# Performance work log

Measured on AMD Instinct MI355X. Metric: run time of the kernel, lower is better.

Reference implementation:

```python
import jax, jax.numpy as jnp
import numpy as np

B, N, H, W = 64, 32, 200, 200


def setup_inputs() -> dict:
    key = jax.random.key(0)
    k1, k2, k3, k4 = jax.random.split(key, 4)
    return {
        "parameter": jax.random.uniform(k1, (B, N, 3), dtype=jnp.float32),
        "x_start": jax.random.uniform(k2, (), dtype=jnp.float32),
        "y_start": jax.random.uniform(k3, (), dtype=jnp.float32),
        "theta": jax.random.uniform(k4, (), dtype=jnp.float32, minval=-3.14159, maxval=3.14159),
        # learned parameters at their torch init values
        "weights": jnp.eye(2, dtype=jnp.float32),
        "biases": jnp.zeros(2, dtype=jnp.float32),
        "thick_mult": jnp.array(0.5, dtype=jnp.float32),
        "thick_bias": jnp.array(0.1, dtype=jnp.float32),
        "dark_exp": jnp.array(1.0, dtype=jnp.float32),
        "dark_non_lin_weight": jnp.array(0.5, dtype=jnp.float32),
        "x_m": jnp.array(1.0, dtype=jnp.float32),
        "y_m": jnp.array(1.0, dtype=jnp.float32),
        "x_b": jnp.array(0.0, dtype=jnp.float32),
        "y_b": jnp.array(0.0, dtype=jnp.float32),
        "use_conv": 0,
    }


def reference(parameter, x_start, y_start, theta, weights, biases, thick_mult,
              thick_bias, dark_exp, dark_non_lin_weight, x_m, y_m, x_b, y_b,
              use_conv):
    # torch.flip(traj, dims=(2,)) then traj[:,:,0] *= -1:
    # channel0 (y) = -parameter[...,1], channel1 (x) = parameter[...,0]
    y0 = -parameter[..., 1]
    x0 = parameter[..., 0]
    # rotation about origin (vectorized over batch; identical per-element math)
    c, s = jnp.cos(theta), jnp.sin(theta)
    x_rot = x0 * c + y0 * s
    y_rot = -x0 * s + y0 * c
    yy = y_rot * y_m + y_b + y_start
    xx = x_rot * x_m + x_b + x_start
    traj = jnp.stack([yy, xx], axis=-1)                      # (B,N,2)
    # curve_to_stroke: matmul(weights, curve).T + biases == traj @ weights.T + biases
    strokes = traj @ weights.T + biases                      # (B,N,2)
    thick = (parameter[..., 2] * 2.0 + 0.5) / 64.0           # (B,N)
    # grid_coords: channel0 = row/H, channel1 = col/W
    gy = jnp.arange(H, dtype=strokes.dtype) / H
    gx = jnp.arange(W, dtype=strokes.dtype) / W
    coords = jnp.stack(jnp.meshgrid(gy, gx, indexing='ij'), axis=-1)  # (H,W,2)
    v = strokes[:, :-1, None, None, :]                       # (B,N-1,1,1,2)
    w = strokes[:, 1:, None, None, :]
    p = coords[None, None]                                   # (1,1,H,W,2)
    wv = w - v
    d2 = jnp.sum(wv * wv, axis=-1)                           # (B,N-1,1,1)
    dot = jnp.sum((p - v) * wv, axis=-1) / (d2 + 1e-5)       # (B,N-1,H,W)
    frac = jnp.clip(dot, 0.0, 1.0)
    proj = v + frac[..., None] * wv                          # (B,N-1,H,W,2)
    diff = p - proj
    dist = jnp.sqrt(jnp.sum(diff * diff, axis=-1))           # (B,N-1,H,W)
    th = thick[:, :-1, None, None] * (1.0 - frac) + thick[:, 1:, None, None] * frac
    th = jnp.maximum(th * thick_mult + thick_bias, 1e-8)
    dark = jnp.clip((th - dist) / th, 0.0, 1.0)
    dark = (dark + 1e-4) ** dark_exp
    nl = jax.nn.sigmoid(dark * 16.0 - 8.0)
    dark = dark_non_lin_weight * nl + (1.0 - dark_non_lin_weight) * dark
    return jnp.max(dark, axis=1)                             # (B,H,W)
```

## Files before the change

kernel.cpp:

```cpp
#include <hip/hip_runtime.h>
#include <math.h>

#define B_ 64
#define N_ 32
#define H_ 200
#define W_ 200
#define NSEG (N_ - 1)
#define TS 32
#define NT 7
#define TILE_RAD 0.111f

__global__ __launch_bounds__(256) void stroke_kernel(
    const float* __restrict__ param,
    const float* __restrict__ x_start,
    const float* __restrict__ y_start,
    const float* __restrict__ theta,
    const float* __restrict__ weights,
    const float* __restrict__ biases,
    const float* __restrict__ thick_mult,
    const float* __restrict__ thick_bias,
    const float* __restrict__ dark_exp_p,
    const float* __restrict__ dark_nlw_p,
    const float* __restrict__ x_m_p,
    const float* __restrict__ y_m_p,
    const float* __restrict__ x_b_p,
    const float* __restrict__ y_b_p,
    float* __restrict__ out)
{
    __shared__ float4 s_A[NSEG];
    __shared__ float4 s_B[NSEG];

    const int b    = blockIdx.z;
    const int tid  = threadIdx.x;
    const int lane = tid & 63;

    const float dexp = dark_exp_p[0], dnlw = dark_nlw_p[0];

    float sy = 0.0f, sx = 0.0f, tk = 0.0f;
    const float tm = thick_mult[0], tb = thick_bias[0];
    if (lane < N_) {
        const float thv = theta[0];
        const float c   = __cosf(thv), s = __sinf(thv);
        const float xs  = x_start[0], ys = y_start[0];
        const float W00 = weights[0], W01 = weights[1];
        const float W10 = weights[2], W11 = weights[3];
        const float bb0 = biases[0],  bb1 = biases[1];
        const float xm  = x_m_p[0], ym = y_m_p[0];
        const float xb  = x_b_p[0], yb = y_b_p[0];
        float p0 = param[(b * N_ + lane) * 3 + 0];
        float p1 = param[(b * N_ + lane) * 3 + 1];
        float p2 = param[(b * N_ + lane) * 3 + 2];
        float x0 = p0, y0 = -p1;
        float x_rot =  x0 * c + y0 * s;
        float y_rot = -x0 * s + y0 * c;
        float yy = y_rot * ym + yb + ys;
        float xx = x_rot * xm + xb + xs;
        sy = yy * W00 + xx * W01 + bb0;
        sx = yy * W10 + xx * W11 + bb1;
        tk = (p2 * 2.0f + 0.5f) * (1.0f / 64.0f);
    }
    float sy1 = __shfl_down(sy, 1);
    float sx1 = __shfl_down(sx, 1);
    float tk1 = __shfl_down(tk, 1);

    bool keep = false;
    float4 A4 = make_float4(0,0,0,0), B4 = make_float4(0,0,0,0);
    if (lane < NSEG) {
        float wvy = sy1 - sy, wvx = sx1 - sx;
        float d2 = wvy * wvy + wvx * wvx;
        float inv_d2 = 1.0f / (d2 + 1e-5f);
        float c0 = tk * tm + tb;
        float c1 = (tk1 - tk) * tm;
        A4 = make_float4(sy, sx, wvy, wvx);
        B4 = make_float4(inv_d2, c0, c1, wvx * inv_d2 * (1.0f / W_));
        const float cy = ((float)(blockIdx.y * TS) + 15.5f) * (1.0f / H_);
        const float cx = ((float)(blockIdx.x * TS) + 15.5f) * (1.0f / W_);
        float dyc = cy - sy, dxc = cx - sx;
        float dot = (dyc * wvy + dxc * wvx) * inv_d2;
        float fr  = __builtin_amdgcn_fmed3f(dot, 0.0f, 1.0f);
        float ey  = dyc - fr * wvy;
        float ex  = dxc - fr * wvx;
        float e2c = ey * ey + ex * ex;
        float thmax = fmaxf(fmaxf(c0, c0 + c1), 1e-8f);
        float reach = thmax + TILE_RAD;
        keep = e2c < reach * reach;
    }
    unsigned long long mask = __ballot(keep);
    const int cnt = (int)__popcll(mask);
    if (keep) {
        int pos = (int)__popcll(mask & ((1ull << lane) - 1ull));
        s_A[pos] = A4; s_B[pos] = B4;
    }
    asm volatile("s_waitcnt lgkmcnt(0)" ::: "memory");

    const int ii = tid >> 4, jj = tid & 15;
    const int r0 = blockIdx.y * TS + ii;
    const int c0 = blockIdx.x * TS + (jj << 1);
    const float py0 = (float)r0 * (1.0f / H_);
    const float py1 = py0 + 16.0f / H_;
    const float px0 = (float)c0 * (1.0f / W_);
    const float px1 = px0 + 1.0f / W_;

    const bool hoist = (dexp > 0.0f) && (dnlw >= 0.0f) && (dnlw <= 1.0f);

    float r00, r01, r10, r11;
    if (hoist) {
        float q00 = INFINITY, q01 = INFINITY, q10 = INFINITY, q11 = INFINITY;
        if (cnt > 0) {
            float4 A = s_A[0], Bc = s_B[0];
            for (int n = 0; n < cnt; ++n) {
                int np = (n + 1 < cnt) ? n + 1 : n;
                float4 An = s_A[np], Bn = s_B[np];
                float dy0 = py0 - A.x, dy1 = py1 - A.x;
                float dx0 = px0 - A.y, dx1 = px1 - A.y;
                float dot00 = fmaf(dy0, A.z, dx0 * A.w) * Bc.x;
                float ddy   = (A.z * Bc.x) * (16.0f / H_);
                float dot01 = dot00 + Bc.w;
                float dot10 = dot00 + ddy;
                float dot11 = dot10 + Bc.w;
                #define PX(dotv, dyv, dxv, qm) { \
                    float fr = __builtin_amdgcn_fmed3f(dotv, 0.0f, 1.0f); \
                    float ey = fmaf(-fr, A.z, dyv); \
                    float ex = fmaf(-fr, A.w, dxv); \
                    float e2 = fmaf(ey, ey, ex * ex); \
                    float th = fmaxf(fmaf(fr, Bc.z, Bc.y), 1e-8f); \
                    float it = __builtin_amdgcn_rcpf(th); \
                    qm = fminf(qm, (e2 * it) * it); }
                PX(dot00, dy0, dx0, q00)
                PX(dot01, dy0, dx1, q01)
                PX(dot10, dy1, dx0, q10)
                PX(dot11, dy1, dx1, q11)
                #undef PX
                A = An; Bc = Bn;
            }
        }
        const bool lin = (dexp == 1.0f);
        #define EPI(qm, rr) { \
            float md = fminf(fmaxf(1.0f - __builtin_amdgcn_sqrtf(qm), 0.0f), 1.0f); \
            float d  = lin ? (md + 1e-4f) : __expf(dexp * __logf(md + 1e-4f)); \
            float nl = __builtin_amdgcn_rcpf(1.0f + __expf(8.0f - d * 16.0f)); \
            rr = dnlw * nl + (1.0f - dnlw) * d; }
        EPI(q00, r00) EPI(q01, r01) EPI(q10, r10) EPI(q11, r11)
        #undef EPI
    } else {
        float b00 = -INFINITY, b01 = -INFINITY, b10 = -INFINITY, b11 = -INFINITY;
        if (cnt < NSEG) {
            float d0  = __expf(dexp * __logf(1e-4f));
            float nl0 = __builtin_amdgcn_rcpf(1.0f + __expf(8.0f - d0 * 16.0f));
            float t0  = dnlw * nl0 + (1.0f - dnlw) * d0;
            b00 = b01 = b10 = b11 = t0;
        }
        for (int n = 0; n < cnt; ++n) {
            float4 A = s_A[n], Bc = s_B[n];
            float dy0 = py0 - A.x, dy1 = py1 - A.x;
            float dx0 = px0 - A.y, dx1 = px1 - A.y;
            float dot00 = fmaf(dy0, A.z, dx0 * A.w) * Bc.x;
            float ddy   = (A.z * Bc.x) * (16.0f / H_);
            float dot01 = dot00 + Bc.w;
            float dot10 = dot00 + ddy;
            float dot11 = dot10 + Bc.w;
            #define PXF(dotv, dyv, dxv, bb) { \
                float fr = __builtin_amdgcn_fmed3f(dotv, 0.0f, 1.0f); \
                float ey = fmaf(-fr, A.z, dyv); \
                float ex = fmaf(-fr, A.w, dxv); \
                float dist = __builtin_amdgcn_sqrtf(fmaf(ey, ey, ex * ex)); \
                float th = fmaxf(fmaf(fr, Bc.z, Bc.y), 1e-8f); \
                float dark = fminf(fmaxf(fmaf(-dist, __builtin_amdgcn_rcpf(th), 1.0f), 0.0f), 1.0f); \
                float d  = __expf(dexp * __logf(dark + 1e-4f)); \
                float nl = __builtin_amdgcn_rcpf(1.0f + __expf(8.0f - d * 16.0f)); \
                bb = fmaxf(bb, dnlw * nl + (1.0f - dnlw) * d); }
            PXF(dot00, dy0, dx0, b00)
            PXF(dot01, dy0, dx1, b01)
            PXF(dot10, dy1, dx0, b10)
            PXF(dot11, dy1, dx1, b11)
            #undef PXF
        }
        r00 = b00; r01 = b01; r10 = b10; r11 = b11;
    }

    if (c0 < W_) {
        if (r0 < H_)
            *reinterpret_cast<float2*>(&out[(b * H_ + r0) * W_ + c0]) = make_float2(r00, r01);
        int r1 = r0 + 16;
        if (r1 < H_)
            *reinterpret_cast<float2*>(&out[(b * H_ + r1) * W_ + c0]) = make_float2(r10, r11);
    }
}

extern "C" void kernel_launch(void* const* d_in, const int* in_sizes, int n_in,
                              void* d_out, int out_size, void* d_ws, size_t ws_size,
                              hipStream_t stream) {
    const float* param      = (const float*)d_in[0];
    const float* x_start    = (const float*)d_in[1];
    const float* y_start    = (const float*)d_in[2];
    const float* theta      = (const float*)d_in[3];
    const float* weights    = (const float*)d_in[4];
    const float* biases     = (const float*)d_in[5];
    const float* thick_mult = (const float*)d_in[6];
    const float* thick_bias = (const float*)d_in[7];
    const float* dark_exp   = (const float*)d_in[8];
    const float* dark_nlw   = (const float*)d_in[9];
    const float* x_m        = (const float*)d_in[10];
    const float* y_m        = (const float*)d_in[11];
    const float* x_b        = (const float*)d_in[12];
    const float* y_b        = (const float*)d_in[13];
    float* out = (float*)d_out;

    dim3 block(256);
    dim3 grid(NT, NT, B_);
    stroke_kernel<<<grid, block, 0, stream>>>(
        param, x_start, y_start, theta, weights, biases,
        thick_mult, thick_bias, dark_exp, dark_nlw,
        x_m, y_m, x_b, y_b, out);
}
```

Measured before the change: 15.59 us.

## Shrink tiles to 32x16 with 128 threads and 1x4 pixels per thread

Changes the tile from 32x32 with 256 threads to 32x16 with 128 threads. Each thread now computes four horizontally adjacent pixels and writes them with one float4 store. The smaller tile radius lets per-tile segment culling reject more segments, so the inner loop does less work. In exchange there are almost twice as many blocks, so the per-block segment setup and culling overhead is repeated more often.

```diff
diff --git a/kernel.cpp b/kernel.cpp
--- a/kernel.cpp
+++ b/kernel.cpp
@@ -6,11 +6,13 @@
 #define H_ 200
 #define W_ 200
 #define NSEG (N_ - 1)
-#define TS 32
-#define NT 7
-#define TILE_RAD 0.111f
-
-__global__ __launch_bounds__(256) void stroke_kernel(
+#define TSX 32
+#define TSY 16
+#define NTX 7
+#define NTY 13
+#define TILE_RAD 0.087f
+
+__global__ __launch_bounds__(128) void stroke_kernel(
     const float* __restrict__ param,
     const float* __restrict__ x_start,
     const float* __restrict__ y_start,
@@ -73,8 +75,8 @@
         float c1 = (tk1 - tk) * tm;
         A4 = make_float4(sy, sx, wvy, wvx);
         B4 = make_float4(inv_d2, c0, c1, wvx * inv_d2 * (1.0f / W_));
-        const float cy = ((float)(blockIdx.y * TS) + 15.5f) * (1.0f / H_);
-        const float cx = ((float)(blockIdx.x * TS) + 15.5f) * (1.0f / W_);
+        const float cy = ((float)(blockIdx.y * TSY) + 7.5f)  * (1.0f / H_);
+        const float cx = ((float)(blockIdx.x * TSX) + 15.5f) * (1.0f / W_);
         float dyc = cy - sy, dxc = cx - sx;
         float dot = (dyc * wvy + dxc * wvx) * inv_d2;
         float fr  = __builtin_amdgcn_fmed3f(dot, 0.0f, 1.0f);
@@ -93,43 +95,44 @@
     }
     asm volatile("s_waitcnt lgkmcnt(0)" ::: "memory");
 
-    const int ii = tid >> 4, jj = tid & 15;
-    const int r0 = blockIdx.y * TS + ii;
-    const int c0 = blockIdx.x * TS + (jj << 1);
-    const float py0 = (float)r0 * (1.0f / H_);
-    const float py1 = py0 + 16.0f / H_;
+    const int ii = tid >> 3;
+    const int jj = tid & 7;
+    const int r  = blockIdx.y * TSY + ii;
+    const int c0 = blockIdx.x * TSX + (jj << 2);
+    const float py  = (float)r  * (1.0f / H_);
     const float px0 = (float)c0 * (1.0f / W_);
-    const float px1 = px0 + 1.0f / W_;
 
     const bool hoist = (dexp > 0.0f) && (dnlw >= 0.0f) && (dnlw <= 1.0f);
 
-    float r00, r01, r10, r11;
+    float o0, o1, o2, o3;
     if (hoist) {
-        float q00 = INFINITY, q01 = INFINITY, q10 = INFINITY, q11 = INFINITY;
+        float q0 = INFINITY, q1 = INFINITY, q2 = INFINITY, q3 = INFINITY;
         if (cnt > 0) {
             float4 A = s_A[0], Bc = s_B[0];
             for (int n = 0; n < cnt; ++n) {
                 int np = (n + 1 < cnt) ? n + 1 : n;
                 float4 An = s_A[np], Bn = s_B[np];
-                float dy0 = py0 - A.x, dy1 = py1 - A.x;
-                float dx0 = px0 - A.y, dx1 = px1 - A.y;
-                float dot00 = fmaf(dy0, A.z, dx0 * A.w) * Bc.x;
-                float ddy   = (A.z * Bc.x) * (16.0f / H_);
-                float dot01 = dot00 + Bc.w;
-                float dot10 = dot00 + ddy;
-                float dot11 = dot10 + Bc.w;
-                #define PX(dotv, dyv, dxv, qm) { \
+                float dy  = py  - A.x;
+                float dx0 = px0 - A.y;
+                float dx1 = dx0 + 1.0f / W_;
+                float dx2 = dx0 + 2.0f / W_;
+                float dx3 = dx0 + 3.0f / W_;
+                float dot0 = fmaf(dy, A.z, dx0 * A.w) * Bc.x;
+                float dot1 = dot0 + Bc.w;
+                float dot2 = dot1 + Bc.w;
+                float dot3 = dot2 + Bc.w;
+                #define PX(dotv, dxv, qm) { \
                     float fr = __builtin_amdgcn_fmed3f(dotv, 0.0f, 1.0f); \
-                    float ey = fmaf(-fr, A.z, dyv); \
+                    float ey = fmaf(-fr, A.z, dy); \
                     float ex = fmaf(-fr, A.w, dxv); \
                     float e2 = fmaf(ey, ey, ex * ex); \
                     float th = fmaxf(fmaf(fr, Bc.z, Bc.y), 1e-8f); \
                     float it = __builtin_amdgcn_rcpf(th); \
                     qm = fminf(qm, (e2 * it) * it); }
-                PX(dot00, dy0, dx0, q00)
-                PX(dot01, dy0, dx1, q01)
-                PX(dot10, dy1, dx0, q10)
-                PX(dot11, dy1, dx1, q11)
+                PX(dot0, dx0, q0)
+                PX(dot1, dx1, q1)
+                PX(dot2, dx2, q2)
+                PX(dot3, dx3, q3)
                 #undef PX
                 A = An; Bc = Bn;
             }
@@ -140,28 +143,30 @@
             float d  = lin ? (md + 1e-4f) : __expf(dexp * __logf(md + 1e-4f)); \
             float nl = __builtin_amdgcn_rcpf(1.0f + __expf(8.0f - d * 16.0f)); \
             rr = dnlw * nl + (1.0f - dnlw) * d; }
-        EPI(q00, r00) EPI(q01, r01) EPI(q10, r10) EPI(q11, r11)
+        EPI(q0, o0) EPI(q1, o1) EPI(q2, o2) EPI(q3, o3)
         #undef EPI
     } else {
-        float b00 = -INFINITY, b01 = -INFINITY, b10 = -INFINITY, b11 = -INFINITY;
+        float b0 = -INFINITY, b1 = -INFINITY, b2 = -INFINITY, b3 = -INFINITY;
         if (cnt < NSEG) {
             float d0  = __expf(dexp * __logf(1e-4f));
             float nl0 = __builtin_amdgcn_rcpf(1.0f + __expf(8.0f - d0 * 16.0f));
             float t0  = dnlw * nl0 + (1.0f - dnlw) * d0;
-            b00 = b01 = b10 = b11 = t0;
+            b0 = b1 = b2 = b3 = t0;
         }
         for (int n = 0; n < cnt; ++n) {
             float4 A = s_A[n], Bc = s_B[n];
-            float dy0 = py0 - A.x, dy1 = py1 - A.x;
-            float dx0 = px0 - A.y, dx1 = px1 - A.y;
-            float dot00 = fmaf(dy0, A.z, dx0 * A.w) * Bc.x;
-            float ddy   = (A.z * Bc.x) * (16.0f / H_);
-            float dot01 = dot00 + Bc.w;
-            float dot10 = dot00 + ddy;
-            float dot11 = dot10 + Bc.w;
-            #define PXF(dotv, dyv, dxv, bb) { \
+            float dy  = py  - A.x;
+            float dx0 = px0 - A.y;
+            float dx1 = dx0 + 1.0f / W_;
+            float dx2 = dx0 + 2.0f / W_;
+            float dx3 = dx0 + 3.0f / W_;
+            float dot0 = fmaf(dy, A.z, dx0 * A.w) * Bc.x;
+            float dot1 = dot0 + Bc.w;
+            float dot2 = dot1 + Bc.w;
+            float dot3 = dot2 + Bc.w;
+            #define PXF(dotv, dxv, bb) { \
                 float fr = __builtin_amdgcn_fmed3f(dotv, 0.0f, 1.0f); \
-                float ey = fmaf(-fr, A.z, dyv); \
+                float ey = fmaf(-fr, A.z, dy); \
                 float ex = fmaf(-fr, A.w, dxv); \
                 float dist = __builtin_amdgcn_sqrtf(fmaf(ey, ey, ex * ex)); \
                 float th = fmaxf(fmaf(fr, Bc.z, Bc.y), 1e-8f); \
@@ -169,21 +174,18 @@
                 float d  = __expf(dexp * __logf(dark + 1e-4f)); \
                 float nl = __builtin_amdgcn_rcpf(1.0f + __expf(8.0f - d * 16.0f)); \
                 bb = fmaxf(bb, dnlw * nl + (1.0f - dnlw) * d); }
-            PXF(dot00, dy0, dx0, b00)
-            PXF(dot01, dy0, dx1, b01)
-            PXF(dot10, dy1, dx0, b10)
-            PXF(dot11, dy1, dx1, b11)
+            PXF(dot0, dx0, b0)
+            PXF(dot1, dx1, b1)
+            PXF(dot2, dx2, b2)
+            PXF(dot3, dx3, b3)
             #undef PXF
         }
-        r00 = b00; r01 = b01; r10 = b10; r11 = b11;
-    }
-
-    if (c0 < W_) {
-        if (r0 < H_)
-            *reinterpret_cast<float2*>(&out[(b * H_ + r0) * W_ + c0]) = make_float2(r00, r01);
-        int r1 = r0 + 16;
-        if (r1 < H_)
-            *reinterpret_cast<float2*>(&out[(b * H_ + r1) * W_ + c0]) = make_float2(r10, r11);
+        o0 = b0; o1 = b1; o2 = b2; o3 = b3;
+    }
+
+    if (r < H_ && c0 < W_) {
+        *reinterpret_cast<float4*>(&out[(b * H_ + r) * W_ + c0]) =
+            make_float4(o0, o1, o2, o3);
     }
 }
 
@@ -206,8 +208,8 @@
     const float* y_b        = (const float*)d_in[13];
     float* out = (float*)d_out;
 
-    dim3 block(256);
-    dim3 grid(NT, NT, B_);
+    dim3 block(128);
+    dim3 grid(NTX, NTY, B_);
     stroke_kernel<<<grid, block, 0, stream>>>(
         param, x_start, y_start, theta, weights, biases,
         thick_mult, thick_bias, dark_exp, dark_nlw,
```

Result: faster. 14.12 us (-9.4%).
